# Optimization experiments

Hardware: AMD Instinct MI355X
Metric: run time of the kernel (lower is better)

Reference implementation:

```python
import jax, jax.numpy as jnp
import numpy as np

P, B, L = 32, 64, 128
E, HB, HP = 64, 128, 128   # byte emb dim, byte GRU hidden, packet GRU hidden
PE = 2 * HB                # packet embedding dim = 256
LH = 128                   # attention linear hidden
NC = 10                    # num classes


def _gru_dir(x, w_ih, w_hh, b_ih, b_hh, reverse=False):
    # x: [T, N, E_in] -> outputs [T, N, H]; PyTorch GRU gate math, h0 = 0.
    H = w_hh.shape[1]
    xg = jnp.einsum('tne,ge->tng', x, w_ih) + b_ih  # precompute input gates [T,N,3H]
    if reverse:
        xg = xg[::-1]

    def step(h, xgt):
        hg = h @ w_hh.T + b_hh
        xr, xz, xn = jnp.split(xgt, 3, axis=-1)
        hr, hz, hn = jnp.split(hg, 3, axis=-1)
        r = jax.nn.sigmoid(xr + hr)
        z = jax.nn.sigmoid(xz + hz)
        n = jnp.tanh(xn + r * hn)
        h = (1.0 - z) * n + z * h
        return h, h

    h0 = jnp.zeros((x.shape[1], H), x.dtype)
    _, ys = jax.lax.scan(step, h0, xg)
    if reverse:
        ys = ys[::-1]
    return ys


def _bigru(x, wif, whf, bif, bhf, wib, whb, bib, bhb):
    f = _gru_dir(x, wif, whf, bif, bhf, reverse=False)
    b = _gru_dir(x, wib, whb, bib, bhb, reverse=True)
    return jnp.concatenate([f, b], axis=-1)


def setup_inputs() -> dict:
    key = jax.random.key(0)
    ks = jax.random.split(key, 32)
    rn = lambda k, shp: (jax.random.normal(k, shp, dtype=jnp.float32) * 0.05)
    inp = {}
    inp['flow'] = jax.random.randint(ks[0], (P, B, L), 0, 256, dtype=jnp.int64)
    inp['emb'] = rn(ks[1], (256, E))
    # byte biGRU (forward / backward dirs)
    inp['byte_wih_f'] = rn(ks[2], (3 * HB, E)); inp['byte_whh_f'] = rn(ks[3], (3 * HB, HB))
    inp['byte_bih_f'] = rn(ks[4], (3 * HB,));   inp['byte_bhh_f'] = rn(ks[5], (3 * HB,))
    inp['byte_wih_b'] = rn(ks[6], (3 * HB, E)); inp['byte_whh_b'] = rn(ks[7], (3 * HB, HB))
    inp['byte_bih_b'] = rn(ks[8], (3 * HB,));   inp['byte_bhh_b'] = rn(ks[9], (3 * HB,))
    # packet biGRU
    inp['pkt_wih_f'] = rn(ks[10], (3 * HP, PE)); inp['pkt_whh_f'] = rn(ks[11], (3 * HP, HP))
    inp['pkt_bih_f'] = rn(ks[12], (3 * HP,));    inp['pkt_bhh_f'] = rn(ks[13], (3 * HP,))
    inp['pkt_wih_b'] = rn(ks[14], (3 * HP, PE)); inp['pkt_whh_b'] = rn(ks[15], (3 * HP, HP))
    inp['pkt_bih_b'] = rn(ks[16], (3 * HP,));    inp['pkt_bhh_b'] = rn(ks[17], (3 * HP,))
    # byte attention (Linear(2HB->LH), Linear(LH->1))
    inp['ba_w1'] = rn(ks[18], (LH, 2 * HB)); inp['ba_b1'] = rn(ks[19], (LH,))
    inp['ba_w2'] = rn(ks[20], (1, LH));      inp['ba_b2'] = rn(ks[21], (1,))
    # packet attention (Linear(2HP->LH), Linear(LH->1))
    inp['pa_w1'] = rn(ks[22], (LH, 2 * HP)); inp['pa_b1'] = rn(ks[23], (LH,))
    inp['pa_w2'] = rn(ks[24], (1, LH));      inp['pa_b2'] = rn(ks[25], (1,))
    # final classifier
    inp['wf'] = rn(ks[26], (NC, 2 * HP)); inp['bf'] = rn(ks[27], (NC,))
    return inp


def reference(flow, emb,
              byte_wih_f, byte_whh_f, byte_bih_f, byte_bhh_f,
              byte_wih_b, byte_whh_b, byte_bih_b, byte_bhh_b,
              pkt_wih_f, pkt_whh_f, pkt_bih_f, pkt_bhh_f,
              pkt_wih_b, pkt_whh_b, pkt_bih_b, pkt_bhh_b,
              ba_w1, ba_b1, ba_w2, ba_b2,
              pa_w1, pa_b1, pa_w2, pa_b2,
              wf, bf):
    p, b, l = flow.shape
    x = emb[flow]                                   # [P,B,L,E]
    # batch the per-packet byte GRU across packets: [L, P*B, E]
    xb = x.transpose(2, 0, 1, 3).reshape(l, p * b, E)
    out = _bigru(xb, byte_wih_f, byte_whh_f, byte_bih_f, byte_bhh_f,
                 byte_wih_b, byte_whh_b, byte_bih_b, byte_bhh_b)  # [L, P*B, 2HB]
    out = out.reshape(l, p, b, 2 * HB)
    # Attention: tanh(lin1) -> lin2 -> softmax over dim=1 of the [L,B,1] view,
    # i.e. over the batch axis (faithful to the original code).
    h = jnp.tanh(jnp.einsum('lpbd,hd->lpbh', out, ba_w1) + ba_b1)
    score = jnp.einsum('lpbh,oh->lpbo', h, ba_w2) + ba_b2          # [L,P,B,1]
    attn = jax.nn.softmax(score, axis=2)
    packet_emb = (out * attn).sum(axis=0)                          # [P,B,2HB]
    # packet biGRU over packet sequence
    out2 = _bigru(packet_emb, pkt_wih_f, pkt_whh_f, pkt_bih_f, pkt_bhh_f,
                  pkt_wih_b, pkt_whh_b, pkt_bih_b, pkt_bhh_b)      # [P,B,2HP]
    h2 = jnp.tanh(jnp.einsum('pbd,hd->pbh', out2, pa_w1) + pa_b1)
    score2 = jnp.einsum('pbh,oh->pbo', h2, pa_w2) + pa_b2          # [P,B,1]
    attn2 = jax.nn.softmax(score2, axis=1)
    flow_emb = (out2 * attn2).sum(axis=1)                          # [P,2HP] (faithful sum over dim=1)
    return flow_emb @ wf.T + bf                                    # [P,NC]
```

## Files before the change

### kernel.cpp

```cpp
#include <hip/hip_runtime.h>
#include <hip/hip_bf16.h>
#include <hip/hip_fp16.h>
#include <cstdint>
#include <cstddef>


#define DINLINE __device__ __forceinline__

typedef _Float16 f16;
typedef f16 f16x8 __attribute__((ext_vector_type(8)));
typedef float f32x4 __attribute__((ext_vector_type(4)));

#define SCL_RZ (-1.44269504089f)
#define SCL_N (2.88539008178f)

static DINLINE float fast_tanh(float x) {
    const float e = __builtin_amdgcn_exp2f(2.88539008178f * x);
    return 1.0f - 2.0f * __builtin_amdgcn_rcpf(1.0f + e);
}

static DINLINE void lds_barrier() {
    asm volatile("s_waitcnt lgkmcnt(0)\n\ts_barrier" ::: "memory");
    __builtin_amdgcn_sched_barrier(0);
}

__global__ void k_tables_w1(const float* __restrict__ emb,
                            const float* __restrict__ wihF, const float* __restrict__ bihF,
                            const float* __restrict__ bhhF,
                            const float* __restrict__ wihB, const float* __restrict__ bihB,
                            const float* __restrict__ bhhB,
                            float4* __restrict__ tab4F, float4* __restrict__ tab4B,
                            const float* __restrict__ w1, f16* __restrict__ w1h,
                            const float* __restrict__ pwihF, const float* __restrict__ pwihB,
                            float* __restrict__ wihTpF, float* __restrict__ wihTpB) {
    if (blockIdx.x >= 640) {
        const int bid = blockIdx.x - 640;
        const int m = bid / 96, bx = bid % 96;
        const float* __restrict__ s = m ? pwihB : pwihF;
        float* __restrict__ d = m ? wihTpB : wihTpF;
        for (int idx = bx * 384 + threadIdx.x; idx < 384 * 256; idx += 96 * 384) {
            const int r = idx >> 8, c = idx & 255;
            d[c * 384 + r] = s[idx];
        }
        return;
    }
    if (blockIdx.x >= 512) {
        const int col = blockIdx.x - 512;
        const int k = threadIdx.x;
        if (k < 256)
            w1h[col * 256 + (k ^ ((col & 7) << 3))] =
                (f16)(SCL_N * w1[col * 256 + k]);
        return;
    }
    const int v = blockIdx.x & 255;
    const int dir = blockIdx.x >> 8;
    const float* wih = dir ? wihB : wihF;
    const float* bih = dir ? bihB : bihF;
    const float* bhh = dir ? bhhB : bhhF;
    float4* tab4 = dir ? tab4B : tab4F;
    __shared__ float er[64];
    __shared__ float sh[384];
    if (threadIdx.x < 64) er[threadIdx.x] = emb[v * 64 + threadIdx.x];
    __syncthreads();
    const int g = threadIdx.x;
    float acc = bih[g] + (g < 256 ? bhh[g] : 0.0f);
    #pragma unroll
    for (int e = 0; e < 64; ++e) acc = fmaf(wih[g * 64 + e], er[e], acc);
    sh[g] = acc * (g < 256 ? SCL_RZ : SCL_N);
    __syncthreads();
    if (g < 128) {
        float4 pk;
        pk.x = sh[g];
        pk.y = sh[g + 128];
        pk.z = sh[g + 256];
        pk.w = 0.f;
        tab4[v * 128 + g] = pk;
    }
}

__global__ __launch_bounds__(512, 1) void k_byte_gru(
    const int* __restrict__ flow,
    const float4* __restrict__ tab4F, const float4* __restrict__ tab4B,
    const float* __restrict__ whhF, const float* __restrict__ whhB,
    const float* __restrict__ bhhF, const float* __restrict__ bhhB,
    __half* __restrict__ hF, __half* __restrict__ hB) {
    const int dir = blockIdx.x & 1;
    const int chunk = blockIdx.x >> 1;
    const int row0 = chunk * 16;
    const int tid = threadIdx.x;
    const int wid = tid >> 6;
    const int lane = tid & 63;
    const int c = lane & 15;
    const int q = lane >> 4;
    const int j = wid * 16 + c;

    const char* __restrict__ t4j =
        reinterpret_cast<const char*>(dir ? tab4B : tab4F) + (j << 4);
    const float* __restrict__ whh = dir ? whhB : whhF;
    const float* __restrict__ bhh = dir ? bhhB : bhhF;
    __half* __restrict__ hout = dir ? hB : hF;

    __shared__ f16 hbuf[2][16 * 128];
    __shared__ int flow_lds[128][16];

    for (int i = tid; i < 16 * 128; i += 512) {
        const int row = i >> 7, t = i & 127;
        flow_lds[t][row] = (flow[row0 * 128 + i] & 255) << 11;
    }
    for (int i = tid; i < 16 * 128; i += 512) hbuf[0][i] = (f16)0.f;

    f16x8 Bf[3][4];
    #pragma unroll
    for (int g = 0; g < 3; ++g) {
        const float scl = (g == 2) ? SCL_N : SCL_RZ;
        #pragma unroll
        for (int ks = 0; ks < 4; ++ks) {
            const float* src = whh + (size_t)(g * 128 + j) * 128 + ks * 32 + q * 8;
            f16x8 b;
            #pragma unroll
            for (int e = 0; e < 8; ++e) b[e] = (f16)(scl * src[e]);
            Bf[g][ks] = b;
        }
    }
    const float bh2 = SCL_N * bhh[j + 256];
    float hold[4];
    #pragma unroll
    for (int rr = 0; rr < 4; ++rr) hold[rr] = 0.f;

    const int tt0 = dir ? 127 : 0;
    __half* hp = hout + ((size_t)tt0 * 2048 + row0 + q * 4) * 128 + j;
    const ptrdiff_t hstep = (dir ? -1 : 1) * (ptrdiff_t)2048 * 128;
    __syncthreads();

    for (int t = 0; t < 128; ++t) {
        const int curb = t & 1, nxtb = curb ^ 1;
        const int tt = dir ? (127 - t) : t;

        const int4 off4 = *reinterpret_cast<const int4*>(&flow_lds[tt][q * 4]);
        float4 x4[4];
        x4[0] = *reinterpret_cast<const float4*>(t4j + off4.x);
        x4[1] = *reinterpret_cast<const float4*>(t4j + off4.y);
        x4[2] = *reinterpret_cast<const float4*>(t4j + off4.z);
        x4[3] = *reinterpret_cast<const float4*>(t4j + off4.w);

        f16x8 Af[4];
        #pragma unroll
        for (int ks = 0; ks < 4; ++ks) {
            const int kb = ks * 32 + q * 8;
            const int idx = c * 128 + (kb ^ ((c & 7) << 3));
            Af[ks] = *reinterpret_cast<const f16x8*>(&hbuf[curb][idx]);
        }

        f32x4 a0 = {0.f, 0.f, 0.f, 0.f};
        f32x4 a1 = {0.f, 0.f, 0.f, 0.f};
        f32x4 a2 = {0.f, 0.f, 0.f, 0.f};
        #pragma unroll
        for (int ks = 0; ks < 4; ++ks) {
            a0 = __builtin_amdgcn_mfma_f32_16x16x32_f16(Af[ks], Bf[0][ks], a0, 0, 0, 0);
            a1 = __builtin_amdgcn_mfma_f32_16x16x32_f16(Af[ks], Bf[1][ks], a1, 0, 0, 0);
            a2 = __builtin_amdgcn_mfma_f32_16x16x32_f16(Af[ks], Bf[2][ks], a2, 0, 0, 0);
        }

        #pragma unroll
        for (int rr = 0; rr < 4; ++rr) {
            const float e0 = __builtin_amdgcn_exp2f(x4[rr].x + a0[rr]);
            const float rg = __builtin_amdgcn_rcpf(1.0f + e0);
            const float e1 = __builtin_amdgcn_exp2f(x4[rr].y + a1[rr]);
            const float zg = __builtin_amdgcn_rcpf(1.0f + e1);
            const float e2 =
                __builtin_amdgcn_exp2f(x4[rr].z + rg * (a2[rr] + bh2));
            const float ng = fmaf(-2.0f, __builtin_amdgcn_rcpf(1.0f + e2), 1.0f);
            const float hn = fmaf(zg, hold[rr] - ng, ng);
            hold[rr] = hn;
            const int row = q * 4 + rr;
            hbuf[nxtb][row * 128 + (j ^ ((row & 7) << 3))] = (f16)hn;
            hp[rr * 128] = (__half)hn;
        }
        hp += hstep;
        lds_barrier();
    }
}

__global__ __launch_bounds__(256, 1) void k_scores_attn(
    const __half* __restrict__ hF, const __half* __restrict__ hB,
    const f16* __restrict__ w1h,
    const float* __restrict__ b1, const float* __restrict__ w2,
    const float* __restrict__ b2, float* __restrict__ attn) {
    __shared__ f16 w1lds[128 * 256];
    __shared__ float sc[128];
    const int tid = threadIdx.x;
    {
        const uint2* src = reinterpret_cast<const uint2*>(w1h);
        uint2* dst = reinterpret_cast<uint2*>(w1lds);
        for (int i = tid; i < 8192; i += 256) dst[i] = src[i];
    }
    const int lane = tid & 63, w = tid >> 6;
    const int c = lane & 15, q = lane >> 4;

    float b1v[8], w2v[8];
    #pragma unroll
    for (int ct = 0; ct < 8; ++ct) {
        b1v[ct] = SCL_N * b1[ct * 16 + c];
        w2v[ct] = w2[ct * 16 + c];
    }
    const float b2v = b2[0];
    __syncthreads();

    for (int it = 0; it < 2; ++it) {
        const int pos0 = blockIdx.x * 256 + it * 128;

        f16x8 Af[2][8];
        #pragma unroll
        for (int pt = 0; pt < 2; ++pt) {
            const size_t pos = (size_t)pos0 + (w * 2 + pt) * 16 + c;
            const f16* hFp = (const f16*)(hF + pos * 128);
            const f16* hBp = (const f16*)(hB + pos * 128);
            #pragma unroll
            for (int ks = 0; ks < 4; ++ks)
                Af[pt][ks] = *reinterpret_cast<const f16x8*>(hFp + ks * 32 + q * 8);
            #pragma unroll
            for (int ks = 0; ks < 4; ++ks)
                Af[pt][4 + ks] = *reinterpret_cast<const f16x8*>(hBp + ks * 32 + q * 8);
        }

        float s[2][4] = {{0.f, 0.f, 0.f, 0.f}, {0.f, 0.f, 0.f, 0.f}};
        #pragma unroll
        for (int ct = 0; ct < 8; ++ct) {
            const int jj = ct * 16 + c;
            f16x8 Bfr[8];
            #pragma unroll
            for (int ks = 0; ks < 8; ++ks) {
                const int k = ks * 32 + q * 8;
                Bfr[ks] = *reinterpret_cast<const f16x8*>(
                    &w1lds[jj * 256 + (k ^ ((jj & 7) << 3))]);
            }
            #pragma unroll
            for (int pt = 0; pt < 2; ++pt) {
                f32x4 acc = {0.f, 0.f, 0.f, 0.f};
                #pragma unroll
                for (int ks = 0; ks < 8; ++ks)
                    acc = __builtin_amdgcn_mfma_f32_16x16x32_f16(Af[pt][ks],
                                                                 Bfr[ks], acc,
                                                                 0, 0, 0);
                #pragma unroll
                for (int rr = 0; rr < 4; ++rr) {
                    const float e2 = __builtin_amdgcn_exp2f(acc[rr] + b1v[ct]);
                    const float th =
                        fmaf(-2.0f, __builtin_amdgcn_rcpf(1.0f + e2), 1.0f);
                    s[pt][rr] = fmaf(w2v[ct], th, s[pt][rr]);
                }
            }
        }
        #pragma unroll
        for (int pt = 0; pt < 2; ++pt) {
            #pragma unroll
            for (int rr = 0; rr < 4; ++rr) {
                float v = s[pt][rr];
                v += __shfl_xor(v, 1);
                v += __shfl_xor(v, 2);
                v += __shfl_xor(v, 4);
                v += __shfl_xor(v, 8);
                if (c == 0) sc[(w * 2 + pt) * 16 + q * 4 + rr] = v + b2v;
            }
        }
        __syncthreads();
        if (tid < 128) {
            const float sv = sc[tid];
            float m = sv;
            for (int off = 32; off; off >>= 1) m = fmaxf(m, __shfl_xor(m, off));
            const float e = __expf(sv - m);
            float sum = e;
            for (int off = 32; off; off >>= 1) sum += __shfl_xor(sum, off);
            attn[pos0 + tid] = e / sum;
        }
        __syncthreads();
    }
}

__global__ __launch_bounds__(256) void k_packet_emb(
    const __half* __restrict__ hF, const __half* __restrict__ hB,
    const float* __restrict__ attn, float* __restrict__ pe) {
    const int tid = threadIdx.x;
    const int w = tid >> 6;
    const int lane = tid & 63;
    const int n = blockIdx.x * 2 + (w >> 1);
    const int l0 = (w & 1) * 64;
    const bool isF = lane < 32;
    const int chunk = lane & 31;
    const __half* __restrict__ hsrc = (isF ? hF : hB) + (size_t)n * 128 + chunk * 4;
    float acc0 = 0.f, acc1 = 0.f, acc2 = 0.f, acc3 = 0.f;
    for (int lb = 0; lb < 64; lb += 8) {
        float wv[8];
        uint2 u[8];
        #pragma unroll
        for (int k = 0; k < 8; ++k) {
            const int l = l0 + lb + k;
            wv[k] = attn[l * 2048 + n];
            u[k] = *reinterpret_cast<const uint2*>(hsrc + (size_t)l * 2048 * 128);
        }
        #pragma unroll
        for (int k = 0; k < 8; ++k) {
            const f16* hv = reinterpret_cast<const f16*>(&u[k]);
            acc0 = fmaf(wv[k], (float)hv[0], acc0);
            acc1 = fmaf(wv[k], (float)hv[1], acc1);
            acc2 = fmaf(wv[k], (float)hv[2], acc2);
            acc3 = fmaf(wv[k], (float)hv[3], acc3);
        }
    }
    __shared__ float4 part[4][64];
    part[w][lane] = (float4){acc0, acc1, acc2, acc3};
    __syncthreads();
    if ((w & 1) == 0) {
        const float4 a = part[w][lane];
        const float4 b = part[w + 1][lane];
        float4 o = {a.x + b.x, a.y + b.y, a.z + b.z, a.w + b.w};
        *reinterpret_cast<float4*>(&pe[n * 256 + (isF ? 0 : 128) + chunk * 4]) = o;
    }
}

__global__ __launch_bounds__(384) void k_pkt_xg(
    const float* __restrict__ pe, const float* __restrict__ wihTF,
    const float* __restrict__ bihF, const float* __restrict__ bhhF,
    const float* __restrict__ wihTB, const float* __restrict__ bihB,
    const float* __restrict__ bhhB, float4* __restrict__ xg4F,
    float4* __restrict__ xg4B) {
    const int dir = blockIdx.y;
    const float* __restrict__ wihT = dir ? wihTB : wihTF;
    const float* __restrict__ bih = dir ? bihB : bihF;
    const float* __restrict__ bhh = dir ? bhhB : bhhF;
    float4* __restrict__ xg4 = dir ? xg4B : xg4F;
    const int rbase = blockIdx.x * 8;
    __shared__ float xrow[8][256];
    __shared__ float sh[8][384];
    for (int i = threadIdx.x; i < 8 * 256; i += 384)
        xrow[i >> 8][i & 255] = pe[rbase * 256 + i];
    __syncthreads();
    const int g = threadIdx.x;
    float acc[8];
    const float bias = bih[g] + (g < 256 ? bhh[g] : 0.0f);
    #pragma unroll
    for (int r = 0; r < 8; ++r) acc[r] = bias;
    for (int d = 0; d < 256; ++d) {
        const float w = wihT[d * 384 + g];
        #pragma unroll
        for (int r = 0; r < 8; ++r) acc[r] = fmaf(w, xrow[r][d], acc[r]);
    }
    const float scl = (g < 256) ? SCL_RZ : SCL_N;
    #pragma unroll
    for (int r = 0; r < 8; ++r) sh[r][g] = scl * acc[r];
    __syncthreads();
    for (int i = threadIdx.x; i < 8 * 128; i += 384) {
        const int r = i >> 7, jj = i & 127;
        float4 pk;
        pk.x = sh[r][jj];
        pk.y = sh[r][jj + 128];
        pk.z = sh[r][jj + 256];
        pk.w = 0.f;
        xg4[(size_t)(rbase + r) * 128 + jj] = pk;
    }
}

__global__ __launch_bounds__(512, 1) void k_pkt_gru(
    const float4* __restrict__ xg4F, const float4* __restrict__ xg4B,
    const float* __restrict__ whhF, const float* __restrict__ whhB,
    const float* __restrict__ bhhF, const float* __restrict__ bhhB,
    float* __restrict__ h2F, float* __restrict__ h2B) {
    const int dir = blockIdx.x & 1;
    const int chunk = blockIdx.x >> 1;
    const int row0 = chunk * 4;
    const int tid = threadIdx.x;
    const int wid = tid >> 6;
    const int lane = tid & 63;
    const int c = lane & 15;
    const int q = lane >> 4;
    const int j = wid * 16 + c;

    const float4* __restrict__ xg4 = dir ? xg4B : xg4F;
    const float* __restrict__ whh = dir ? whhB : whhF;
    const float* __restrict__ bhh = dir ? bhhB : bhhF;
    float* __restrict__ hout = dir ? h2B : h2F;

    __shared__ f16 hbuf[2][16 * 128];

    {
        f16* hb = reinterpret_cast<f16*>(hbuf);
        for (int i = tid; i < 2 * 16 * 128; i += 512) hb[i] = (f16)0.f;
    }

    f16x8 Bf[3][4];
    #pragma unroll
    for (int g = 0; g < 3; ++g) {
        const float scl = (g == 2) ? SCL_N : SCL_RZ;
        #pragma unroll
        for (int ks = 0; ks < 4; ++ks) {
            const float* src = whh + (size_t)(g * 128 + j) * 128 + ks * 32 + q * 8;
            f16x8 b;
            #pragma unroll
            for (int e = 0; e < 8; ++e) b[e] = (f16)(scl * src[e]);
            Bf[g][ks] = b;
        }
    }
    const float bh2 = SCL_N * bhh[j + 256];
    float hold = 0.f;
    const int slot = q * 4;
    __syncthreads();

    for (int t = 0; t < 32; ++t) {
        const int curb = t & 1, nxtb = curb ^ 1;
        const int tt = dir ? (31 - t) : t;

        const float4 x4 = xg4[(size_t)(tt * 64 + row0 + q) * 128 + j];

        f16x8 Af[4];
        #pragma unroll
        for (int ks = 0; ks < 4; ++ks) {
            const int kb = ks * 32 + q * 8;
            const int idx = c * 128 + (kb ^ ((c & 7) << 3));
            Af[ks] = *reinterpret_cast<const f16x8*>(&hbuf[curb][idx]);
        }

        f32x4 a0 = {0.f, 0.f, 0.f, 0.f};
        f32x4 a1 = {0.f, 0.f, 0.f, 0.f};
        f32x4 a2 = {0.f, 0.f, 0.f, 0.f};
        #pragma unroll
        for (int ks = 0; ks < 4; ++ks) {
            a0 = __builtin_amdgcn_mfma_f32_16x16x32_f16(Af[ks], Bf[0][ks], a0, 0, 0, 0);
            a1 = __builtin_amdgcn_mfma_f32_16x16x32_f16(Af[ks], Bf[1][ks], a1, 0, 0, 0);
            a2 = __builtin_amdgcn_mfma_f32_16x16x32_f16(Af[ks], Bf[2][ks], a2, 0, 0, 0);
        }

        {
            const float e0 = __builtin_amdgcn_exp2f(x4.x + a0[0]);
            const float rg = __builtin_amdgcn_rcpf(1.0f + e0);
            const float e1 = __builtin_amdgcn_exp2f(x4.y + a1[0]);
            const float zg = __builtin_amdgcn_rcpf(1.0f + e1);
            const float e2 = __builtin_amdgcn_exp2f(x4.z + rg * (a2[0] + bh2));
            const float ng = fmaf(-2.0f, __builtin_amdgcn_rcpf(1.0f + e2), 1.0f);
            const float hn = fmaf(zg, hold - ng, ng);
            hold = hn;
            hbuf[nxtb][slot * 128 + (j ^ ((slot & 7) << 3))] = (f16)hn;
            hout[((size_t)tt * 64 + row0 + q) * 128 + j] = hn;
        }
        lds_barrier();
    }
}

__global__ __launch_bounds__(128) void k_scores2(
    const float* __restrict__ h2F, const float* __restrict__ h2B,
    const float* __restrict__ paw1,
    const float* __restrict__ pab1, const float* __restrict__ paw2,
    const float* __restrict__ pab2, float* __restrict__ scores2) {
    const int n = blockIdx.x;
    const int tid = threadIdx.x;
    __shared__ float x[256];
    __shared__ float red[2];
    x[tid] = h2F[n * 128 + tid];
    x[tid + 128] = h2B[n * 128 + tid];
    __syncthreads();
    float acc = pab1[tid];
    const float* wr = paw1 + tid * 256;
    #pragma unroll 8
    for (int d = 0; d < 256; ++d) acc = fmaf(wr[d], x[d], acc);
    float s = paw2[tid] * fast_tanh(acc);
    s += __shfl_xor(s, 1);
    s += __shfl_xor(s, 2);
    s += __shfl_xor(s, 4);
    s += __shfl_xor(s, 8);
    s += __shfl_xor(s, 16);
    s += __shfl_xor(s, 32);
    if ((tid & 63) == 0) red[tid >> 6] = s;
    __syncthreads();
    if (tid == 0) scores2[n] = red[0] + red[1] + pab2[0];
}

__global__ __launch_bounds__(256) void k_final3(
    const float* __restrict__ h2F, const float* __restrict__ h2B,
    const float* __restrict__ scores2, const float* __restrict__ wf,
    const float* __restrict__ bfv, float* __restrict__ outp) {
    const int p = blockIdx.x;
    const int tid = threadIdx.x;
    __shared__ float sc[64];
    __shared__ float femb[256];
    __shared__ float red[64];

    if (tid < 64) {
        const float s = scores2[p * 64 + tid];
        float m = s;
        for (int off = 32; off; off >>= 1) m = fmaxf(m, __shfl_xor(m, off));
        const float e = __expf(s - m);
        float sum = e;
        for (int off = 32; off; off >>= 1) sum += __shfl_xor(sum, off);
        sc[tid] = e / sum;
    }
    __syncthreads();

    {
        const float* __restrict__ hsrc = (tid < 128) ? h2F : h2B;
        const int d = tid & 127;
        float acc = 0.f;
        for (int b = 0; b < 64; ++b)
            acc = fmaf(sc[b], hsrc[(p * 64 + b) * 128 + d], acc);
        femb[tid] = acc;
    }
    __syncthreads();

    const float fv = femb[tid];
    #pragma unroll
    for (int c = 0; c < 10; ++c) {
        float s = fv * wf[c * 256 + tid];
        s += __shfl_xor(s, 1);
        s += __shfl_xor(s, 2);
        s += __shfl_xor(s, 4);
        s += __shfl_xor(s, 8);
        s += __shfl_xor(s, 16);
        s += __shfl_xor(s, 32);
        if ((tid & 63) == 0) red[(c << 2) | (tid >> 6)] = s;
        __syncthreads();
        if (tid == 0)
            outp[p * 10 + c] = bfv[c] + red[c << 2] + red[(c << 2) | 1] +
                               red[(c << 2) | 2] + red[(c << 2) | 3];
        __syncthreads();
    }
}

extern "C" void kernel_launch(void* const* d_in, const int* in_sizes, int n_in,
                              void* d_out, int out_size, void* d_ws,
                              size_t ws_size, hipStream_t stream) {
    const int* flow = (const int*)d_in[0];
    const float* emb = (const float*)d_in[1];
    const float* byte_wih_f = (const float*)d_in[2];
    const float* byte_whh_f = (const float*)d_in[3];
    const float* byte_bih_f = (const float*)d_in[4];
    const float* byte_bhh_f = (const float*)d_in[5];
    const float* byte_wih_b = (const float*)d_in[6];
    const float* byte_whh_b = (const float*)d_in[7];
    const float* byte_bih_b = (const float*)d_in[8];
    const float* byte_bhh_b = (const float*)d_in[9];
    const float* pkt_wih_f = (const float*)d_in[10];
    const float* pkt_whh_f = (const float*)d_in[11];
    const float* pkt_bih_f = (const float*)d_in[12];
    const float* pkt_bhh_f = (const float*)d_in[13];
    const float* pkt_wih_b = (const float*)d_in[14];
    const float* pkt_whh_b = (const float*)d_in[15];
    const float* pkt_bih_b = (const float*)d_in[16];
    const float* pkt_bhh_b = (const float*)d_in[17];
    const float* ba_w1 = (const float*)d_in[18];
    const float* ba_b1 = (const float*)d_in[19];
    const float* ba_w2 = (const float*)d_in[20];
    const float* ba_b2 = (const float*)d_in[21];
    const float* pa_w1 = (const float*)d_in[22];
    const float* pa_b1 = (const float*)d_in[23];
    const float* pa_w2 = (const float*)d_in[24];
    const float* pa_b2 = (const float*)d_in[25];
    const float* wf = (const float*)d_in[26];
    const float* bf = (const float*)d_in[27];

    char* base = (char*)d_ws;
    size_t off = 0;
    auto allocf = [&](size_t nf) -> float* {
        float* p = (float*)(base + off);
        off += nf * sizeof(float);
        return p;
    };
    auto alloch = [&](size_t nh) -> __half* {
        off = (off + 255) & ~(size_t)255;
        __half* p = (__half*)(base + off);
        off += nh * sizeof(__half);
        return p;
    };
    float* wihTpF = allocf(256 * 384);
    float* wihTpB = allocf(256 * 384);
    float* attn = allocf(262144);
    float* pe = allocf(2048 * 256);
    float4* tab4F = (float4*)allocf(256 * 128 * 4);
    float4* tab4B = (float4*)allocf(256 * 128 * 4);
    float4* xg4F = (float4*)allocf((size_t)2048 * 128 * 4);
    float4* xg4B = (float4*)allocf((size_t)2048 * 128 * 4);
    float* h2F = allocf(32 * 64 * 128);
    float* h2B = allocf(32 * 64 * 128);
    float* scores2 = allocf(2048);
    __half* w1h = alloch(128 * 256);
    __half* hF = alloch((size_t)128 * 2048 * 128);
    __half* hB = alloch((size_t)128 * 2048 * 128);
    if (off > ws_size) return;
    (void)in_sizes; (void)n_in; (void)out_size;

    k_tables_w1<<<832, 384, 0, stream>>>(emb, byte_wih_f, byte_bih_f,
                                         byte_bhh_f, byte_wih_b, byte_bih_b,
                                         byte_bhh_b, tab4F, tab4B, ba_w1,
                                         (f16*)w1h, pkt_wih_f, pkt_wih_b,
                                         wihTpF, wihTpB);

    k_byte_gru<<<256, 512, 0, stream>>>(flow, tab4F, tab4B, byte_whh_f,
                                        byte_whh_b, byte_bhh_f, byte_bhh_b, hF,
                                        hB);

    k_scores_attn<<<1024, 256, 0, stream>>>(hF, hB, (const f16*)w1h, ba_b1,
                                            ba_w2, ba_b2, attn);
    k_packet_emb<<<1024, 256, 0, stream>>>(hF, hB, attn, pe);

    k_pkt_xg<<<dim3(256, 2), 384, 0, stream>>>(pe, wihTpF, pkt_bih_f,
                                               pkt_bhh_f, wihTpB, pkt_bih_b,
                                               pkt_bhh_b, xg4F, xg4B);
    k_pkt_gru<<<32, 512, 0, stream>>>(xg4F, xg4B, pkt_whh_f, pkt_whh_b,
                                      pkt_bhh_f, pkt_bhh_b, h2F, h2B);
    k_scores2<<<2048, 128, 0, stream>>>(h2F, h2B, pa_w1, pa_b1, pa_w2, pa_b2,
                                        scores2);
    k_final3<<<32, 256, 0, stream>>>(h2F, h2B, scores2, wf, bf, (float*)d_out);
}
```

Baseline: 273.8 us.

## Fuse packet attention scores into final kernel and retile packet-emb and xg kernels

Removes the separate k_scores2 launch by computing the packet-level attention scores inside k_final3, with each of 32 blocks handling 64 packets' scores. k_packet_emb now assigns one sequence row per block and splits the L reduction across four waves. k_pkt_xg processes 16 rows per block to reuse each weight load more. The fusion cuts a launch and an intermediate buffer but concentrates the score GEMV onto only 32 blocks, which reduces parallelism substantially.

Measured after the change: 834.8 us. 205% more time.

```diff
diff --git a/kernel.cpp b/kernel.cpp
--- a/kernel.cpp
+++ b/kernel.cpp
@@ -283,13 +283,13 @@
     const int tid = threadIdx.x;
     const int w = tid >> 6;
     const int lane = tid & 63;
-    const int n = blockIdx.x * 2 + (w >> 1);
-    const int l0 = (w & 1) * 64;
+    const int n = blockIdx.x;
+    const int l0 = w * 32;
     const bool isF = lane < 32;
     const int chunk = lane & 31;
     const __half* __restrict__ hsrc = (isF ? hF : hB) + (size_t)n * 128 + chunk * 4;
     float acc0 = 0.f, acc1 = 0.f, acc2 = 0.f, acc3 = 0.f;
-    for (int lb = 0; lb < 64; lb += 8) {
+    for (int lb = 0; lb < 32; lb += 8) {
         float wv[8];
         uint2 u[8];
         #pragma unroll
@@ -310,10 +310,13 @@
     __shared__ float4 part[4][64];
     part[w][lane] = (float4){acc0, acc1, acc2, acc3};
     __syncthreads();
-    if ((w & 1) == 0) {
-        const float4 a = part[w][lane];
-        const float4 b = part[w + 1][lane];
-        float4 o = {a.x + b.x, a.y + b.y, a.z + b.z, a.w + b.w};
+    if (w == 0) {
+        const float4 a = part[0][lane];
+        const float4 b = part[1][lane];
+        const float4 cc = part[2][lane];
+        const float4 d = part[3][lane];
+        float4 o = {a.x + b.x + cc.x + d.x, a.y + b.y + cc.y + d.y,
+                    a.z + b.z + cc.z + d.z, a.w + b.w + cc.w + d.w};
         *reinterpret_cast<float4*>(&pe[n * 256 + (isF ? 0 : 128) + chunk * 4]) = o;
     }
 }
@@ -329,27 +332,27 @@
     const float* __restrict__ bih = dir ? bihB : bihF;
     const float* __restrict__ bhh = dir ? bhhB : bhhF;
     float4* __restrict__ xg4 = dir ? xg4B : xg4F;
-    const int rbase = blockIdx.x * 8;
-    __shared__ float xrow[8][256];
-    __shared__ float sh[8][384];
-    for (int i = threadIdx.x; i < 8 * 256; i += 384)
+    const int rbase = blockIdx.x * 16;
+    __shared__ float xrow[16][256];
+    __shared__ float sh[16][384];
+    for (int i = threadIdx.x; i < 16 * 256; i += 384)
         xrow[i >> 8][i & 255] = pe[rbase * 256 + i];
     __syncthreads();
     const int g = threadIdx.x;
-    float acc[8];
+    float acc[16];
     const float bias = bih[g] + (g < 256 ? bhh[g] : 0.0f);
     #pragma unroll
-    for (int r = 0; r < 8; ++r) acc[r] = bias;
+    for (int r = 0; r < 16; ++r) acc[r] = bias;
     for (int d = 0; d < 256; ++d) {
         const float w = wihT[d * 384 + g];
         #pragma unroll
-        for (int r = 0; r < 8; ++r) acc[r] = fmaf(w, xrow[r][d], acc[r]);
+        for (int r = 0; r < 16; ++r) acc[r] = fmaf(w, xrow[r][d], acc[r]);
     }
     const float scl = (g < 256) ? SCL_RZ : SCL_N;
     #pragma unroll
-    for (int r = 0; r < 8; ++r) sh[r][g] = scl * acc[r];
-    __syncthreads();
-    for (int i = threadIdx.x; i < 8 * 128; i += 384) {
+    for (int r = 0; r < 16; ++r) sh[r][g] = scl * acc[r];
+    __syncthreads();
+    for (int i = threadIdx.x; i < 16 * 128; i += 384) {
         const int r = i >> 7, jj = i & 127;
         float4 pk;
         pk.x = sh[r][jj];
@@ -445,37 +448,11 @@
     }
 }
 
-__global__ __launch_bounds__(128) void k_scores2(
+__global__ __launch_bounds__(256) void k_final3(
     const float* __restrict__ h2F, const float* __restrict__ h2B,
     const float* __restrict__ paw1,
     const float* __restrict__ pab1, const float* __restrict__ paw2,
-    const float* __restrict__ pab2, float* __restrict__ scores2) {
-    const int n = blockIdx.x;
-    const int tid = threadIdx.x;
-    __shared__ float x[256];
-    __shared__ float red[2];
-    x[tid] = h2F[n * 128 + tid];
-    x[tid + 128] = h2B[n * 128 + tid];
-    __syncthreads();
-    float acc = pab1[tid];
-    const float* wr = paw1 + tid * 256;
-    #pragma unroll 8
-    for (int d = 0; d < 256; ++d) acc = fmaf(wr[d], x[d], acc);
-    float s = paw2[tid] * fast_tanh(acc);
-    s += __shfl_xor(s, 1);
-    s += __shfl_xor(s, 2);
-    s += __shfl_xor(s, 4);
-    s += __shfl_xor(s, 8);
-    s += __shfl_xor(s, 16);
-    s += __shfl_xor(s, 32);
-    if ((tid & 63) == 0) red[tid >> 6] = s;
-    __syncthreads();
-    if (tid == 0) scores2[n] = red[0] + red[1] + pab2[0];
-}
-
-__global__ __launch_bounds__(256) void k_final3(
-    const float* __restrict__ h2F, const float* __restrict__ h2B,
-    const float* __restrict__ scores2, const float* __restrict__ wf,
+    const float* __restrict__ pab2, const float* __restrict__ wf,
     const float* __restrict__ bfv, float* __restrict__ outp) {
     const int p = blockIdx.x;
     const int tid = threadIdx.x;
@@ -483,8 +460,38 @@
     __shared__ float femb[256];
     __shared__ float red[64];
 
+    {
+        const int w = tid >> 6, lane = tid & 63;
+        const float b2v = pab2[0];
+        for (int ni = 0; ni < 16; ++ni) {
+            const int n = p * 64 + w * 16 + ni;
+            float acc0 = pab1[lane], acc1 = pab1[lane + 64];
+            const float* x0 = h2F + n * 128;
+            const float* x1 = h2B + n * 128;
+            const float* w0 = paw1 + lane * 256;
+            const float* w1 = paw1 + (lane + 64) * 256;
+            #pragma unroll 4
+            for (int d = 0; d < 128; ++d) {
+                const float xf = x0[d], xb = x1[d];
+                acc0 = fmaf(w0[d], xf, acc0);
+                acc0 = fmaf(w0[d + 128], xb, acc0);
+                acc1 = fmaf(w1[d], xf, acc1);
+                acc1 = fmaf(w1[d + 128], xb, acc1);
+            }
+            float s = fmaf(paw2[lane], fast_tanh(acc0), paw2[lane + 64] * fast_tanh(acc1));
+            s += __shfl_xor(s, 1);
+            s += __shfl_xor(s, 2);
+            s += __shfl_xor(s, 4);
+            s += __shfl_xor(s, 8);
+            s += __shfl_xor(s, 16);
+            s += __shfl_xor(s, 32);
+            if (lane == 0) sc[w * 16 + ni] = s + b2v;
+        }
+    }
+    __syncthreads();
+
     if (tid < 64) {
-        const float s = scores2[p * 64 + tid];
+        const float s = sc[tid];
         float m = s;
         for (int off = 32; off; off >>= 1) m = fmaxf(m, __shfl_xor(m, off));
         const float e = __expf(s - m);
@@ -578,7 +585,6 @@
     float4* xg4B = (float4*)allocf((size_t)2048 * 128 * 4);
     float* h2F = allocf(32 * 64 * 128);
     float* h2B = allocf(32 * 64 * 128);
-    float* scores2 = allocf(2048);
     __half* w1h = alloch(128 * 256);
     __half* hF = alloch((size_t)128 * 2048 * 128);
     __half* hB = alloch((size_t)128 * 2048 * 128);
@@ -597,14 +603,13 @@
 
     k_scores_attn<<<1024, 256, 0, stream>>>(hF, hB, (const f16*)w1h, ba_b1,
                                             ba_w2, ba_b2, attn);
-    k_packet_emb<<<1024, 256, 0, stream>>>(hF, hB, attn, pe);
-
-    k_pkt_xg<<<dim3(256, 2), 384, 0, stream>>>(pe, wihTpF, pkt_bih_f,
+    k_packet_emb<<<2048, 256, 0, stream>>>(hF, hB, attn, pe);
+
+    k_pkt_xg<<<dim3(128, 2), 384, 0, stream>>>(pe, wihTpF, pkt_bih_f,
                                                pkt_bhh_f, wihTpB, pkt_bih_b,
                                                pkt_bhh_b, xg4F, xg4B);
     k_pkt_gru<<<32, 512, 0, stream>>>(xg4F, xg4B, pkt_whh_f, pkt_whh_b,
                                       pkt_bhh_f, pkt_bhh_b, h2F, h2B);
-    k_scores2<<<2048, 128, 0, stream>>>(h2F, h2B, pa_w1, pa_b1, pa_w2, pa_b2,
-                                        scores2);
-    k_final3<<<32, 256, 0, stream>>>(h2F, h2B, scores2, wf, bf, (float*)d_out);
-}
+    k_final3<<<32, 256, 0, stream>>>(h2F, h2B, pa_w1, pa_b1, pa_w2, pa_b2, wf,
+                                     bf, (float*)d_out);
+}
```
